# Optimization experiments

Measured on AMD Instinct MI355X. Metric: run time of the kernel, lower is better.

## Reference

```python
import jax, jax.numpy as jnp
import numpy as np

B, L, DM = 4, 512, 512
NH, DK, DV = 8, 64, 64  # NOTE: module's view puts d_k as the 'heads' axis, n_head as feature axis
EPS = 1e-6


def setup_inputs() -> dict:
    key = jax.random.key(0)
    ks = jax.random.split(key, 12)
    xav = lambda k, shp: jax.random.uniform(k, shp, jnp.float32, -1.0, 1.0) * np.sqrt(6.0 / (shp[0] + shp[1]))
    return {
        "q": jax.random.normal(ks[0], (B, L, DM), jnp.float32),
        "k": jax.random.normal(ks[1], (B, L, DM), jnp.float32),
        "v": jax.random.normal(ks[2], (B, L, DM), jnp.float32),
        "similarity": jax.random.normal(ks[3], (B, DK, L, L), jnp.float32),
        "Wq": xav(ks[4], (NH * DK, DM)),
        "Wk": xav(ks[5], (NH * DK, DM)),
        "Wv": xav(ks[6], (NH * DV, DM)),
        "Wfc": xav(ks[7], (DM, NH * DV)),
        "bfc": jnp.zeros((DM,), jnp.float32),
        "ln_g": jnp.ones((DM,), jnp.float32),
        "ln_b": jnp.zeros((DM,), jnp.float32),
    }


def reference(q, k, v, similarity, Wq, Wk, Wv, Wfc, bfc, ln_g, ln_b):
    b, l, dm = q.shape
    residual = q
    # pre-LayerNorm applied to q only (normalize_before=True)
    mu = jnp.mean(q, axis=-1, keepdims=True)
    var = jnp.mean(jnp.square(q - mu), axis=-1, keepdims=True)
    qn = (q - mu) / jnp.sqrt(var + EPS) * ln_g + ln_b
    # projections, then view(b, l, d_k, n_head).transpose(1,2) -> [b, d_k, l, n_head]
    Q = (qn @ Wq.T).reshape(b, l, DK, NH).transpose(0, 2, 1, 3)
    K = (k @ Wk.T).reshape(b, l, DK, NH).transpose(0, 2, 1, 3)
    V = (v @ Wv.T).reshape(b, l, DK, NH).transpose(0, 2, 1, 3)
    temp = jnp.asarray(DK ** 0.5, q.dtype)
    # bias-augmented scaled dot-product attention: scores [b, d_k, l, l]
    scores = jnp.einsum('bhqe,bhke->bhqk', Q, K) / temp + similarity
    attn = jax.nn.softmax(scores, axis=-1)  # dropout omitted (eval mode)
    out = jnp.einsum('bhqk,bhke->bhqe', attn, V)  # [b, d_k, l, n_head]
    out = out.transpose(0, 2, 1, 3).reshape(b, l, DK * NH)
    out = out @ Wfc.T + bfc + residual
    return out, attn
```

## Files before the change

### kernel.cpp

```cpp
#include <hip/hip_runtime.h>

#define DMODEL 512
#define LSEQ   512
#define BATCH  4
#define NHEAD  8
#define DKH    64

__global__ __launch_bounds__(256) void ln_kernel(const float* __restrict__ q,
    const float* __restrict__ gamma, const float* __restrict__ beta,
    float* __restrict__ qn) {
  int row = blockIdx.x;
  const float* x = q + (size_t)row * DMODEL;
  int t = threadIdx.x;
  float v0 = x[t];
  float v1 = x[t + 256];
  float s  = v0 + v1;
  float ss = v0 * v0 + v1 * v1;
  #pragma unroll
  for (int o = 32; o >= 1; o >>= 1) {
    s  += __shfl_down(s, o);
    ss += __shfl_down(ss, o);
  }
  __shared__ float ls[4], lss[4];
  __shared__ float smu, srstd;
  int wid = t >> 6, lane = t & 63;
  if (lane == 0) { ls[wid] = s; lss[wid] = ss; }
  __syncthreads();
  if (t == 0) {
    float S  = ls[0] + ls[1] + ls[2] + ls[3];
    float SS = lss[0] + lss[1] + lss[2] + lss[3];
    float mu  = S * (1.0f / DMODEL);
    float var = SS * (1.0f / DMODEL) - mu * mu;
    smu = mu;
    srstd = rsqrtf(var + 1e-6f);
  }
  __syncthreads();
  float mu = smu, rstd = srstd;
  float* o = qn + (size_t)row * DMODEL;
  o[t]       = (v0 - mu) * rstd * gamma[t]       + beta[t];
  o[t + 256] = (v1 - mu) * rstd * gamma[t + 256] + beta[t + 256];
}

__device__ __forceinline__ void gemm64_body(const float* __restrict__ A,
    const float* __restrict__ W, float* __restrict__ C,
    const float* __restrict__ bias, const float* __restrict__ resid) {
  __shared__ float As[16][68];
  __shared__ float Ws[16][68];
  const int t = threadIdx.x;
  const int row0 = blockIdx.y * 64, col0 = blockIdx.x * 64;
  const int lr = t >> 2;
  const int lk = (t & 3) << 2;
  const int tx = t & 15, ty = t >> 4;
  float acc[4][4] = {};
  for (int k0 = 0; k0 < DMODEL; k0 += 16) {
    float4 a = *(const float4*)(A + (size_t)(row0 + lr) * DMODEL + k0 + lk);
    float4 w = *(const float4*)(W + (size_t)(col0 + lr) * DMODEL + k0 + lk);
    if (k0) __syncthreads();
    As[lk+0][lr] = a.x; As[lk+1][lr] = a.y; As[lk+2][lr] = a.z; As[lk+3][lr] = a.w;
    Ws[lk+0][lr] = w.x; Ws[lk+1][lr] = w.y; Ws[lk+2][lr] = w.z; Ws[lk+3][lr] = w.w;
    __syncthreads();
    #pragma unroll
    for (int kk = 0; kk < 16; kk++) {
      float4 av = *(const float4*)&As[kk][ty << 2];
      float4 wv = *(const float4*)&Ws[kk][tx << 2];
      float ar[4] = {av.x, av.y, av.z, av.w};
      float wr[4] = {wv.x, wv.y, wv.z, wv.w};
      #pragma unroll
      for (int i = 0; i < 4; i++)
        #pragma unroll
        for (int j = 0; j < 4; j++)
          acc[i][j] = fmaf(ar[i], wr[j], acc[i][j]);
    }
  }
  #pragma unroll
  for (int i = 0; i < 4; i++) {
    int r = row0 + (ty << 2) + i;
    int c = col0 + (tx << 2);
    float4 o = {acc[i][0], acc[i][1], acc[i][2], acc[i][3]};
    if (bias) {
      o.x += bias[c]; o.y += bias[c+1]; o.z += bias[c+2]; o.w += bias[c+3];
    }
    if (resid) {
      float4 rv = *(const float4*)(resid + (size_t)r * DMODEL + c);
      o.x += rv.x; o.y += rv.y; o.z += rv.z; o.w += rv.w;
    }
    *(float4*)(C + (size_t)r * DMODEL + c) = o;
  }
}

__global__ __launch_bounds__(256) void proj_kernel(
    const float* __restrict__ qn, const float* __restrict__ kin, const float* __restrict__ vin,
    const float* __restrict__ Wq, const float* __restrict__ Wk, const float* __restrict__ Wv,
    float* __restrict__ Qp, float* __restrict__ Kp, float* __restrict__ Vp) {
  const float* A; const float* W; float* C;
  if (blockIdx.z == 0)      { A = qn;  W = Wq; C = Qp; }
  else if (blockIdx.z == 1) { A = kin; W = Wk; C = Kp; }
  else                      { A = vin; W = Wv; C = Vp; }
  gemm64_body(A, W, C, nullptr, nullptr);
}

__global__ __launch_bounds__(256) void fc_kernel(
    const float* __restrict__ AO, const float* __restrict__ Wfc,
    const float* __restrict__ bfc, const float* __restrict__ resid,
    float* __restrict__ out) {
  gemm64_body(AO, Wfc, out, bfc, resid);
}

__global__ __launch_bounds__(256) void attn_kernel(
    const float* __restrict__ Qp, const float* __restrict__ Kp, const float* __restrict__ Vp,
    const float* __restrict__ sim, float* __restrict__ attn_out, float* __restrict__ AO) {
  __shared__ float Kt[NHEAD][LSEQ];
  __shared__ float Vt[NHEAD][LSEQ];
  __shared__ float Qt[128][NHEAD];
  const int qt = blockIdx.x, dk = blockIdx.y, b = blockIdx.z;
  const int t = threadIdx.x;
  const float* Kbase = Kp + ((size_t)b * LSEQ) * DMODEL + dk * NHEAD;
  const float* Vbase = Vp + ((size_t)b * LSEQ) * DMODEL + dk * NHEAD;
  for (int idx = t; idx < LSEQ * NHEAD; idx += 256) {
    int l = idx >> 3, j = idx & 7;
    Kt[j][l] = Kbase[(size_t)l * DMODEL + j];
    Vt[j][l] = Vbase[(size_t)l * DMODEL + j];
  }
  const float* Qbase = Qp + ((size_t)b * LSEQ + qt * 128) * DMODEL + dk * NHEAD;
  for (int idx = t; idx < 128 * NHEAD; idx += 256) {
    int l = idx >> 3, j = idx & 7;
    Qt[l][j] = Qbase[(size_t)l * DMODEL + j];
  }
  __syncthreads();

  const int wid = t >> 6, lane = t & 63;
  for (int qi = 0; qi < 32; qi++) {
    const int ql = wid * 32 + qi;
    const int q  = qt * 128 + ql;
    const size_t rowoff = (((size_t)(b * DKH + dk) * LSEQ) + q) * LSEQ;
    const float* simrow = sim + rowoff;
    float sv[8];
    #pragma unroll
    for (int c = 0; c < 8; c++) sv[c] = simrow[c * 64 + lane];
    float qreg[8];
    #pragma unroll
    for (int j = 0; j < 8; j++) qreg[j] = Qt[ql][j];
    float s[8];
    #pragma unroll
    for (int c = 0; c < 8; c++) {
      int kp = c * 64 + lane;
      float d = 0.0f;
      #pragma unroll
      for (int j = 0; j < 8; j++) d = fmaf(qreg[j], Kt[j][kp], d);
      s[c] = d * 0.125f + sv[c];
    }
    float m = s[0];
    #pragma unroll
    for (int c = 1; c < 8; c++) m = fmaxf(m, s[c]);
    #pragma unroll
    for (int o = 1; o < 64; o <<= 1) m = fmaxf(m, __shfl_xor(m, o));
    float e[8]; float sum = 0.0f;
    #pragma unroll
    for (int c = 0; c < 8; c++) { e[c] = __expf(s[c] - m); sum += e[c]; }
    #pragma unroll
    for (int o = 1; o < 64; o <<= 1) sum += __shfl_xor(sum, o);
    const float r = 1.0f / sum;
    float p[8];
    #pragma unroll
    for (int c = 0; c < 8; c++) p[c] = e[c] * r;
    float* arow = attn_out + rowoff;
    #pragma unroll
    for (int c = 0; c < 8; c++) arow[c * 64 + lane] = p[c];
    float pv[8];
    #pragma unroll
    for (int j = 0; j < 8; j++) {
      float acc = 0.0f;
      #pragma unroll
      for (int c = 0; c < 8; c++) acc = fmaf(p[c], Vt[j][c * 64 + lane], acc);
      pv[j] = acc;
    }
    #pragma unroll
    for (int j = 0; j < 8; j++) {
      #pragma unroll
      for (int o = 1; o < 64; o <<= 1) pv[j] += __shfl_xor(pv[j], o);
    }
    if (lane == 0) {
      float* ao = AO + ((size_t)b * LSEQ + q) * DMODEL + dk * NHEAD;
      float4 o0 = {pv[0], pv[1], pv[2], pv[3]};
      float4 o1 = {pv[4], pv[5], pv[6], pv[7]};
      *(float4*)ao = o0;
      *(float4*)(ao + 4) = o1;
    }
  }
}

extern "C" void kernel_launch(void* const* d_in, const int* in_sizes, int n_in,
                              void* d_out, int out_size, void* d_ws, size_t ws_size,
                              hipStream_t stream) {
  const float* q    = (const float*)d_in[0];
  const float* k    = (const float*)d_in[1];
  const float* v    = (const float*)d_in[2];
  const float* sim  = (const float*)d_in[3];
  const float* Wq   = (const float*)d_in[4];
  const float* Wk   = (const float*)d_in[5];
  const float* Wv   = (const float*)d_in[6];
  const float* Wfc  = (const float*)d_in[7];
  const float* bfc  = (const float*)d_in[8];
  const float* ln_g = (const float*)d_in[9];
  const float* ln_b = (const float*)d_in[10];

  float* out  = (float*)d_out;
  float* attn = out + (size_t)BATCH * LSEQ * DMODEL;

  const size_t NTOK = (size_t)BATCH * LSEQ;
  float* qn = (float*)d_ws;
  float* Qp = qn + NTOK * DMODEL;
  float* Kp = Qp + NTOK * DMODEL;
  float* Vp = Kp + NTOK * DMODEL;
  float* AO = qn;

  ln_kernel<<<dim3(NTOK), dim3(256), 0, stream>>>(q, ln_g, ln_b, qn);
  proj_kernel<<<dim3(8, 32, 3), dim3(256), 0, stream>>>(qn, k, v, Wq, Wk, Wv, Qp, Kp, Vp);
  attn_kernel<<<dim3(4, DKH, BATCH), dim3(256), 0, stream>>>(Qp, Kp, Vp, sim, attn, AO);
  fc_kernel<<<dim3(8, 32, 1), dim3(256), 0, stream>>>(AO, Wfc, bfc, q, out);
}
```

Before: 598.6 us.

## Use split-bf16 MFMA GEMMs and register-resident K in attention kernel

Replaces the FP32 SIMT projection and output GEMMs with MFMA bf16 GEMMs that use a hi/lo split (three MFMAs per tile) to keep near-FP32 accuracy. A new conversion kernel pre-splits k, v and all weights into bf16 pairs. The attention kernel now holds K in registers, uses smaller query tiles with more blocks, and vectorises the similarity and attention loads and stores. Intermediate buffers are placed in the output region to save workspace, which adds an extra conversion pass and extra memory traffic.

```diff
diff --git a/kernel.cpp b/kernel.cpp
--- a/kernel.cpp
+++ b/kernel.cpp
@@ -3,12 +3,28 @@
 #define DMODEL 512
 #define LSEQ   512
 #define BATCH  4
-#define NHEAD  8
-#define DKH    64
+#define NTOK   2048
+
+typedef __attribute__((ext_vector_type(8))) short bf8;
+typedef __attribute__((ext_vector_type(4))) float f4;
+typedef __attribute__((ext_vector_type(4))) unsigned short us4;
+typedef __attribute__((ext_vector_type(8))) unsigned short us8;
+
+__device__ __forceinline__ unsigned short bf16_rne(float f) {
+  unsigned int u = __float_as_uint(f);
+  u += 0x7FFFu + ((u >> 16) & 1u);
+  return (unsigned short)(u >> 16);
+}
+__device__ __forceinline__ void split2(float f, unsigned short& h, unsigned short& l) {
+  unsigned short hh = bf16_rne(f);
+  float fh = __uint_as_float(((unsigned int)hh) << 16);
+  h = hh;
+  l = bf16_rne(f - fh);
+}
 
 __global__ __launch_bounds__(256) void ln_kernel(const float* __restrict__ q,
     const float* __restrict__ gamma, const float* __restrict__ beta,
-    float* __restrict__ qn) {
+    unsigned short* __restrict__ qh, unsigned short* __restrict__ qlo) {
   int row = blockIdx.x;
   const float* x = q + (size_t)row * DMODEL;
   int t = threadIdx.x;
@@ -36,155 +52,227 @@
   }
   __syncthreads();
   float mu = smu, rstd = srstd;
-  float* o = qn + (size_t)row * DMODEL;
-  o[t]       = (v0 - mu) * rstd * gamma[t]       + beta[t];
-  o[t + 256] = (v1 - mu) * rstd * gamma[t + 256] + beta[t + 256];
-}
-
-__device__ __forceinline__ void gemm64_body(const float* __restrict__ A,
-    const float* __restrict__ W, float* __restrict__ C,
-    const float* __restrict__ bias, const float* __restrict__ resid) {
-  __shared__ float As[16][68];
-  __shared__ float Ws[16][68];
+  float n0 = (v0 - mu) * rstd * gamma[t]       + beta[t];
+  float n1 = (v1 - mu) * rstd * gamma[t + 256] + beta[t + 256];
+  unsigned short h, l;
+  size_t base = (size_t)row * DMODEL;
+  split2(n0, h, l); qh[base + t] = h;       qlo[base + t] = l;
+  split2(n1, h, l); qh[base + t + 256] = h; qlo[base + t + 256] = l;
+}
+
+__global__ __launch_bounds__(256) void conv_kernel(
+    const float* __restrict__ k, const float* __restrict__ v,
+    const float* __restrict__ Wq, const float* __restrict__ Wk,
+    const float* __restrict__ Wv, const float* __restrict__ Wf,
+    unsigned short* __restrict__ kh, unsigned short* __restrict__ kl,
+    unsigned short* __restrict__ vh, unsigned short* __restrict__ vl,
+    unsigned short* __restrict__ Wqh, unsigned short* __restrict__ Wql,
+    unsigned short* __restrict__ Wkh, unsigned short* __restrict__ Wkl,
+    unsigned short* __restrict__ Wvh, unsigned short* __restrict__ Wvl,
+    unsigned short* __restrict__ Wfh, unsigned short* __restrict__ Wfl) {
+  const float* src; unsigned short* dh; unsigned short* dl; int n;
+  switch (blockIdx.y) {
+    case 0:  src = k;  dh = kh;  dl = kl;  n = NTOK * DMODEL; break;
+    case 1:  src = v;  dh = vh;  dl = vl;  n = NTOK * DMODEL; break;
+    case 2:  src = Wq; dh = Wqh; dl = Wql; n = DMODEL * DMODEL; break;
+    case 3:  src = Wk; dh = Wkh; dl = Wkl; n = DMODEL * DMODEL; break;
+    case 4:  src = Wv; dh = Wvh; dl = Wvl; n = DMODEL * DMODEL; break;
+    default: src = Wf; dh = Wfh; dl = Wfl; n = DMODEL * DMODEL; break;
+  }
+  int idx = blockIdx.x * 1024 + threadIdx.x * 4;
+  if (idx >= n) return;
+  float4 f = *(const float4*)(src + idx);
+  us4 oh, ol;
+  unsigned short h, l;
+  split2(f.x, h, l); oh[0] = h; ol[0] = l;
+  split2(f.y, h, l); oh[1] = h; ol[1] = l;
+  split2(f.z, h, l); oh[2] = h; ol[2] = l;
+  split2(f.w, h, l); oh[3] = h; ol[3] = l;
+  *(us4*)(dh + idx) = oh;
+  *(us4*)(dl + idx) = ol;
+}
+
+__device__ __forceinline__ void mfma_gemm_body(
+    const unsigned short* __restrict__ Ah, const unsigned short* __restrict__ Al,
+    const unsigned short* __restrict__ Wh, const unsigned short* __restrict__ Wl,
+    float* __restrict__ C, const float* __restrict__ bias, const float* __restrict__ resid) {
   const int t = threadIdx.x;
-  const int row0 = blockIdx.y * 64, col0 = blockIdx.x * 64;
-  const int lr = t >> 2;
-  const int lk = (t & 3) << 2;
-  const int tx = t & 15, ty = t >> 4;
-  float acc[4][4] = {};
-  for (int k0 = 0; k0 < DMODEL; k0 += 16) {
-    float4 a = *(const float4*)(A + (size_t)(row0 + lr) * DMODEL + k0 + lk);
-    float4 w = *(const float4*)(W + (size_t)(col0 + lr) * DMODEL + k0 + lk);
-    if (k0) __syncthreads();
-    As[lk+0][lr] = a.x; As[lk+1][lr] = a.y; As[lk+2][lr] = a.z; As[lk+3][lr] = a.w;
-    Ws[lk+0][lr] = w.x; Ws[lk+1][lr] = w.y; Ws[lk+2][lr] = w.z; Ws[lk+3][lr] = w.w;
-    __syncthreads();
-    #pragma unroll
-    for (int kk = 0; kk < 16; kk++) {
-      float4 av = *(const float4*)&As[kk][ty << 2];
-      float4 wv = *(const float4*)&Ws[kk][tx << 2];
-      float ar[4] = {av.x, av.y, av.z, av.w};
-      float wr[4] = {wv.x, wv.y, wv.z, wv.w};
-      #pragma unroll
-      for (int i = 0; i < 4; i++)
-        #pragma unroll
-        for (int j = 0; j < 4; j++)
-          acc[i][j] = fmaf(ar[i], wr[j], acc[i][j]);
-    }
-  }
-  #pragma unroll
-  for (int i = 0; i < 4; i++) {
-    int r = row0 + (ty << 2) + i;
-    int c = col0 + (tx << 2);
-    float4 o = {acc[i][0], acc[i][1], acc[i][2], acc[i][3]};
-    if (bias) {
-      o.x += bias[c]; o.y += bias[c+1]; o.z += bias[c+2]; o.w += bias[c+3];
-    }
-    if (resid) {
-      float4 rv = *(const float4*)(resid + (size_t)r * DMODEL + c);
-      o.x += rv.x; o.y += rv.y; o.z += rv.z; o.w += rv.w;
-    }
-    *(float4*)(C + (size_t)r * DMODEL + c) = o;
-  }
-}
-
-__global__ __launch_bounds__(256) void proj_kernel(
-    const float* __restrict__ qn, const float* __restrict__ kin, const float* __restrict__ vin,
-    const float* __restrict__ Wq, const float* __restrict__ Wk, const float* __restrict__ Wv,
+  const int w = t >> 6, lane = t & 63;
+  const int wm = w >> 1, wn = w & 1;
+  const int r0 = blockIdx.y * 64 + wm * 32;
+  const int c0 = blockIdx.x * 64 + wn * 32;
+  const int lr = lane & 15, quad = lane >> 4;
+  f4 acc[2][2] = {};
+  for (int k0 = 0; k0 < DMODEL; k0 += 32) {
+    const int ko = k0 + quad * 8;
+    bf8 ah[2], al[2], bh[2], bl[2];
+    #pragma unroll
+    for (int mi = 0; mi < 2; mi++) {
+      const size_t off = (size_t)(r0 + mi * 16 + lr) * DMODEL + ko;
+      ah[mi] = *(const bf8*)(Ah + off);
+      al[mi] = *(const bf8*)(Al + off);
+    }
+    #pragma unroll
+    for (int ni = 0; ni < 2; ni++) {
+      const size_t off = (size_t)(c0 + ni * 16 + lr) * DMODEL + ko;
+      bh[ni] = *(const bf8*)(Wh + off);
+      bl[ni] = *(const bf8*)(Wl + off);
+    }
+    #pragma unroll
+    for (int mi = 0; mi < 2; mi++)
+      #pragma unroll
+      for (int ni = 0; ni < 2; ni++) {
+        acc[mi][ni] = __builtin_amdgcn_mfma_f32_16x16x32_bf16(al[mi], bh[ni], acc[mi][ni], 0, 0, 0);
+        acc[mi][ni] = __builtin_amdgcn_mfma_f32_16x16x32_bf16(ah[mi], bl[ni], acc[mi][ni], 0, 0, 0);
+        acc[mi][ni] = __builtin_amdgcn_mfma_f32_16x16x32_bf16(ah[mi], bh[ni], acc[mi][ni], 0, 0, 0);
+      }
+  }
+  #pragma unroll
+  for (int mi = 0; mi < 2; mi++)
+    #pragma unroll
+    for (int ni = 0; ni < 2; ni++)
+      #pragma unroll
+      for (int r = 0; r < 4; r++) {
+        int row = r0 + mi * 16 + quad * 4 + r;
+        int col = c0 + ni * 16 + lr;
+        float o = acc[mi][ni][r];
+        if (bias)  o += bias[col];
+        if (resid) o += resid[(size_t)row * DMODEL + col];
+        C[(size_t)row * DMODEL + col] = o;
+      }
+}
+
+__global__ __launch_bounds__(256) void proj_mfma(
+    const unsigned short* __restrict__ qnh, const unsigned short* __restrict__ qnl,
+    const unsigned short* __restrict__ kh, const unsigned short* __restrict__ kl,
+    const unsigned short* __restrict__ vh, const unsigned short* __restrict__ vl,
+    const unsigned short* __restrict__ Wqh, const unsigned short* __restrict__ Wql,
+    const unsigned short* __restrict__ Wkh, const unsigned short* __restrict__ Wkl,
+    const unsigned short* __restrict__ Wvh, const unsigned short* __restrict__ Wvl,
     float* __restrict__ Qp, float* __restrict__ Kp, float* __restrict__ Vp) {
-  const float* A; const float* W; float* C;
-  if (blockIdx.z == 0)      { A = qn;  W = Wq; C = Qp; }
-  else if (blockIdx.z == 1) { A = kin; W = Wk; C = Kp; }
-  else                      { A = vin; W = Wv; C = Vp; }
-  gemm64_body(A, W, C, nullptr, nullptr);
-}
-
-__global__ __launch_bounds__(256) void fc_kernel(
-    const float* __restrict__ AO, const float* __restrict__ Wfc,
+  const unsigned short *Ah, *Al, *Wh, *Wl; float* C;
+  if (blockIdx.z == 0)      { Ah = qnh; Al = qnl; Wh = Wqh; Wl = Wql; C = Qp; }
+  else if (blockIdx.z == 1) { Ah = kh;  Al = kl;  Wh = Wkh; Wl = Wkl; C = Kp; }
+  else                      { Ah = vh;  Al = vl;  Wh = Wvh; Wl = Wvl; C = Vp; }
+  mfma_gemm_body(Ah, Al, Wh, Wl, C, nullptr, nullptr);
+}
+
+__global__ __launch_bounds__(256) void fc_mfma(
+    const unsigned short* __restrict__ AOh, const unsigned short* __restrict__ AOl,
+    const unsigned short* __restrict__ Wfh, const unsigned short* __restrict__ Wfl,
     const float* __restrict__ bfc, const float* __restrict__ resid,
     float* __restrict__ out) {
-  gemm64_body(AO, Wfc, out, bfc, resid);
-}
-
-__global__ __launch_bounds__(256) void attn_kernel(
+  mfma_gemm_body(AOh, AOl, Wfh, Wfl, out, bfc, resid);
+}
+
+__global__ __launch_bounds__(256, 3) void attn2_kernel(
     const float* __restrict__ Qp, const float* __restrict__ Kp, const float* __restrict__ Vp,
-    const float* __restrict__ sim, float* __restrict__ attn_out, float* __restrict__ AO) {
-  __shared__ float Kt[NHEAD][LSEQ];
-  __shared__ float Vt[NHEAD][LSEQ];
-  __shared__ float Qt[128][NHEAD];
+    const float* __restrict__ sim, float* __restrict__ attn_out,
+    unsigned short* __restrict__ AOh, unsigned short* __restrict__ AOl) {
+  __shared__ float Vt[8][516];
+  __shared__ float Qs[64][8];
   const int qt = blockIdx.x, dk = blockIdx.y, b = blockIdx.z;
   const int t = threadIdx.x;
-  const float* Kbase = Kp + ((size_t)b * LSEQ) * DMODEL + dk * NHEAD;
-  const float* Vbase = Vp + ((size_t)b * LSEQ) * DMODEL + dk * NHEAD;
-  for (int idx = t; idx < LSEQ * NHEAD; idx += 256) {
+  const float* Vbase = Vp + (size_t)b * LSEQ * DMODEL + dk * 8;
+  #pragma unroll
+  for (int it = 0; it < 16; it++) {
+    int idx = it * 256 + t;
     int l = idx >> 3, j = idx & 7;
-    Kt[j][l] = Kbase[(size_t)l * DMODEL + j];
     Vt[j][l] = Vbase[(size_t)l * DMODEL + j];
   }
-  const float* Qbase = Qp + ((size_t)b * LSEQ + qt * 128) * DMODEL + dk * NHEAD;
-  for (int idx = t; idx < 128 * NHEAD; idx += 256) {
+  const float* Qbase = Qp + ((size_t)b * LSEQ + qt * 64) * DMODEL + dk * 8;
+  #pragma unroll
+  for (int it = 0; it < 2; it++) {
+    int idx = it * 256 + t;
     int l = idx >> 3, j = idx & 7;
-    Qt[l][j] = Qbase[(size_t)l * DMODEL + j];
-  }
+    Qs[l][j] = Qbase[(size_t)l * DMODEL + j];
+  }
+  const int lane = t & 63, w = t >> 6;
+  const float* Kbase = Kp + (size_t)b * LSEQ * DMODEL + dk * 8;
+  float Kr[2][8][4];
+  #pragma unroll
+  for (int c = 0; c < 2; c++)
+    #pragma unroll
+    for (int s = 0; s < 4; s++) {
+      const float* kr = Kbase + (size_t)(c * 256 + lane * 4 + s) * DMODEL;
+      float4 a  = *(const float4*)kr;
+      float4 bb = *(const float4*)(kr + 4);
+      Kr[c][0][s] = a.x;  Kr[c][1][s] = a.y;  Kr[c][2][s] = a.z;  Kr[c][3][s] = a.w;
+      Kr[c][4][s] = bb.x; Kr[c][5][s] = bb.y; Kr[c][6][s] = bb.z; Kr[c][7][s] = bb.w;
+    }
   __syncthreads();
 
-  const int wid = t >> 6, lane = t & 63;
-  for (int qi = 0; qi < 32; qi++) {
-    const int ql = wid * 32 + qi;
-    const int q  = qt * 128 + ql;
-    const size_t rowoff = (((size_t)(b * DKH + dk) * LSEQ) + q) * LSEQ;
-    const float* simrow = sim + rowoff;
-    float sv[8];
-    #pragma unroll
-    for (int c = 0; c < 8; c++) sv[c] = simrow[c * 64 + lane];
+  for (int qi = 0; qi < 16; qi++) {
+    const int ql = w * 16 + qi;
+    const int q  = qt * 64 + ql;
+    const size_t rowoff = (((size_t)(b * 64 + dk) * LSEQ) + q) * LSEQ;
+    float4 sv0 = *(const float4*)(sim + rowoff + lane * 4);
+    float4 sv1 = *(const float4*)(sim + rowoff + 256 + lane * 4);
+    float svf[2][4] = {{sv0.x, sv0.y, sv0.z, sv0.w}, {sv1.x, sv1.y, sv1.z, sv1.w}};
     float qreg[8];
     #pragma unroll
-    for (int j = 0; j < 8; j++) qreg[j] = Qt[ql][j];
-    float s[8];
-    #pragma unroll
-    for (int c = 0; c < 8; c++) {
-      int kp = c * 64 + lane;
-      float d = 0.0f;
-      #pragma unroll
-      for (int j = 0; j < 8; j++) d = fmaf(qreg[j], Kt[j][kp], d);
-      s[c] = d * 0.125f + sv[c];
-    }
-    float m = s[0];
-    #pragma unroll
-    for (int c = 1; c < 8; c++) m = fmaxf(m, s[c]);
+    for (int j = 0; j < 8; j++) qreg[j] = Qs[ql][j];
+    float sc[2][4];
+    #pragma unroll
+    for (int c = 0; c < 2; c++)
+      #pragma unroll
+      for (int s = 0; s < 4; s++) {
+        float d = 0.0f;
+        #pragma unroll
+        for (int j = 0; j < 8; j++) d = fmaf(qreg[j], Kr[c][j][s], d);
+        sc[c][s] = fmaf(d, 0.125f, svf[c][s]);
+      }
+    float m = sc[0][0];
+    #pragma unroll
+    for (int c = 0; c < 2; c++)
+      #pragma unroll
+      for (int s = 0; s < 4; s++) m = fmaxf(m, sc[c][s]);
     #pragma unroll
     for (int o = 1; o < 64; o <<= 1) m = fmaxf(m, __shfl_xor(m, o));
-    float e[8]; float sum = 0.0f;
-    #pragma unroll
-    for (int c = 0; c < 8; c++) { e[c] = __expf(s[c] - m); sum += e[c]; }
+    float p[2][4]; float sum = 0.0f;
+    #pragma unroll
+    for (int c = 0; c < 2; c++)
+      #pragma unroll
+      for (int s = 0; s < 4; s++) { p[c][s] = __expf(sc[c][s] - m); sum += p[c][s]; }
     #pragma unroll
     for (int o = 1; o < 64; o <<= 1) sum += __shfl_xor(sum, o);
     const float r = 1.0f / sum;
-    float p[8];
-    #pragma unroll
-    for (int c = 0; c < 8; c++) p[c] = e[c] * r;
-    float* arow = attn_out + rowoff;
-    #pragma unroll
-    for (int c = 0; c < 8; c++) arow[c * 64 + lane] = p[c];
+    #pragma unroll
+    for (int c = 0; c < 2; c++)
+      #pragma unroll
+      for (int s = 0; s < 4; s++) p[c][s] *= r;
+    float4 st0 = {p[0][0], p[0][1], p[0][2], p[0][3]};
+    float4 st1 = {p[1][0], p[1][1], p[1][2], p[1][3]};
+    *(float4*)(attn_out + rowoff + lane * 4) = st0;
+    *(float4*)(attn_out + rowoff + 256 + lane * 4) = st1;
     float pv[8];
     #pragma unroll
     for (int j = 0; j < 8; j++) {
       float acc = 0.0f;
       #pragma unroll
-      for (int c = 0; c < 8; c++) acc = fmaf(p[c], Vt[j][c * 64 + lane], acc);
+      for (int c = 0; c < 2; c++) {
+        float4 vv = *(const float4*)&Vt[j][c * 256 + lane * 4];
+        acc = fmaf(p[c][0], vv.x, acc);
+        acc = fmaf(p[c][1], vv.y, acc);
+        acc = fmaf(p[c][2], vv.z, acc);
+        acc = fmaf(p[c][3], vv.w, acc);
+      }
       pv[j] = acc;
     }
     #pragma unroll
-    for (int j = 0; j < 8; j++) {
+    for (int j = 0; j < 8; j++)
       #pragma unroll
       for (int o = 1; o < 64; o <<= 1) pv[j] += __shfl_xor(pv[j], o);
-    }
-    if (lane == 0) {
-      float* ao = AO + ((size_t)b * LSEQ + q) * DMODEL + dk * NHEAD;
-      float4 o0 = {pv[0], pv[1], pv[2], pv[3]};
-      float4 o1 = {pv[4], pv[5], pv[6], pv[7]};
-      *(float4*)ao = o0;
-      *(float4*)(ao + 4) = o1;
+    if (lane < 2) {
+      us8 ov;
+      #pragma unroll
+      for (int j = 0; j < 8; j++) {
+        unsigned short h, l;
+        split2(pv[j], h, l);
+        ov[j] = (lane == 0) ? h : l;
+      }
+      unsigned short* dst = ((lane == 0) ? AOh : AOl) + ((size_t)b * LSEQ + q) * DMODEL + dk * 8;
+      *(us8*)dst = ov;
     }
   }
 }
@@ -205,17 +293,34 @@
   const float* ln_b = (const float*)d_in[10];
 
   float* out  = (float*)d_out;
-  float* attn = out + (size_t)BATCH * LSEQ * DMODEL;
-
-  const size_t NTOK = (size_t)BATCH * LSEQ;
-  float* qn = (float*)d_ws;
-  float* Qp = qn + NTOK * DMODEL;
-  float* Kp = Qp + NTOK * DMODEL;
-  float* Vp = Kp + NTOK * DMODEL;
-  float* AO = qn;
-
-  ln_kernel<<<dim3(NTOK), dim3(256), 0, stream>>>(q, ln_g, ln_b, qn);
-  proj_kernel<<<dim3(8, 32, 3), dim3(256), 0, stream>>>(qn, k, v, Wq, Wk, Wv, Qp, Kp, Vp);
-  attn_kernel<<<dim3(4, DKH, BATCH), dim3(256), 0, stream>>>(Qp, Kp, Vp, sim, attn, AO);
-  fc_kernel<<<dim3(8, 32, 1), dim3(256), 0, stream>>>(AO, Wfc, bfc, q, out);
-}
+  float* attn = out + (size_t)NTOK * DMODEL;
+
+  unsigned short* kh = (unsigned short*)attn;
+  unsigned short* kl = kh + (size_t)NTOK * DMODEL;
+  unsigned short* vh = kl + (size_t)NTOK * DMODEL;
+  unsigned short* vl = vh + (size_t)NTOK * DMODEL;
+  float* Qp = out;
+
+  unsigned short* qnh = (unsigned short*)d_ws;
+  unsigned short* qnl = qnh + (size_t)NTOK * DMODEL;
+  unsigned short* Wqh = qnl + (size_t)NTOK * DMODEL;
+  unsigned short* Wql = Wqh + DMODEL * DMODEL;
+  unsigned short* Wkh = Wql + DMODEL * DMODEL;
+  unsigned short* Wkl = Wkh + DMODEL * DMODEL;
+  unsigned short* Wvh = Wkl + DMODEL * DMODEL;
+  unsigned short* Wvl = Wvh + DMODEL * DMODEL;
+  unsigned short* Wfh = Wvl + DMODEL * DMODEL;
+  unsigned short* Wfl = Wfh + DMODEL * DMODEL;
+  float* Kp = (float*)(Wfl + DMODEL * DMODEL);
+  float* Vp = Kp + (size_t)NTOK * DMODEL;
+  unsigned short* AOh = qnh;
+  unsigned short* AOl = qnl;
+
+  ln_kernel<<<dim3(NTOK), dim3(256), 0, stream>>>(q, ln_g, ln_b, qnh, qnl);
+  conv_kernel<<<dim3(1024, 6), dim3(256), 0, stream>>>(k, v, Wq, Wk, Wv, Wfc,
+      kh, kl, vh, vl, Wqh, Wql, Wkh, Wkl, Wvh, Wvl, Wfh, Wfl);
+  proj_mfma<<<dim3(8, 32, 3), dim3(256), 0, stream>>>(qnh, qnl, kh, kl, vh, vl,
+      Wqh, Wql, Wkh, Wkl, Wvh, Wvl, Qp, Kp, Vp);
+  attn2_kernel<<<dim3(8, 64, 4), dim3(256), 0, stream>>>(Qp, Kp, Vp, sim, attn, AOh, AOl);
+  fc_mfma<<<dim3(8, 32, 1), dim3(256), 0, stream>>>(AOh, AOl, Wfh, Wfl, bfc, q, out);
+}
```

Result: faster. 584.5 us (-2.4%).
